# Performance work log

Hardware: AMD Instinct MI355X
Metric: run time of the kernel (lower is better)

The kernel has to match this reference:

```python
import jax, jax.numpy as jnp
import numpy as np

N = 100000
E = 3200000
D = 256
K = 1024
BETA = 1.0
LAMBDA_GRAPH = 0.1
ALPHA = 0.5
NUM_ITER = 2
LN_EPS = 1e-5


def setup_inputs() -> dict:
    key = jax.random.key(0)
    k1, k2, k3 = jax.random.split(key, 3)
    x = jax.random.normal(k1, (N, D), dtype=jnp.float32)
    edge_index = jax.random.randint(k2, (2, E), 0, N, dtype=jnp.int64)
    memory = jax.random.normal(k3, (K, D), dtype=jnp.float32) * 0.02  # memory patterns M [K, d]
    ln_gamma = jnp.ones((D,), dtype=jnp.float32)
    ln_beta = jnp.zeros((D,), dtype=jnp.float32)
    return {"x": x, "edge_index": edge_index, "memory": memory,
            "ln_gamma": ln_gamma, "ln_beta": ln_beta}


def _layer_norm(x, gamma, beta):
    mu = jnp.mean(x, axis=-1, keepdims=True)
    var = jnp.mean(jnp.square(x - mu), axis=-1, keepdims=True)
    return (x - mu) * jax.lax.rsqrt(var + LN_EPS) * gamma + beta


def _laplacian_term(x, row, col):
    # symmetric normalized Laplacian: x - D^{-1/2} A D^{-1/2} x
    deg = jax.ops.segment_sum(jnp.ones((E,), x.dtype), col, num_segments=N)  # [N]
    deg_inv_sqrt = jnp.where(deg > 0, jax.lax.rsqrt(jnp.maximum(deg, 1.0)), 0.0)
    norm_x = deg_inv_sqrt[:, None] * x                                        # [N, d]
    agg = jax.ops.segment_sum(norm_x[col], row, num_segments=N)               # scatter-add
    return x - deg_inv_sqrt[:, None] * agg


def reference(x, edge_index, memory, ln_gamma, ln_beta):
    row, col = edge_index[0], edge_index[1]
    lap_coeff = 2.0 * LAMBDA_GRAPH
    for _ in range(NUM_ITER):
        # Hopfield retrieval: softmax(beta * x M^T) M
        attn = jax.nn.softmax(BETA * jnp.einsum('nd,kd->nk', x, memory), axis=-1)
        retrieved = jnp.einsum('nk,kd->nd', attn, memory)
        lap = _laplacian_term(x, row, col)
        x_new = (1.0 - ALPHA) * x + ALPHA * (retrieved - lap_coeff * lap)
        x = _layer_norm(x_new, ln_gamma, ln_beta)
    return x
```

## Files before the change

### kernel.cpp

```cpp
#include <hip/hip_runtime.h>

#define DD 256
#define BSHIFT 9
#define BROWS  512
#define NBMAX  1024

typedef short bf16x8 __attribute__((ext_vector_type(8)));
typedef float f32x4 __attribute__((ext_vector_type(4)));

__device__ __forceinline__ float bf2f(ushort v) {
    union { uint u; float f; } c; c.u = ((uint)v) << 16; return c.f;
}
__device__ __forceinline__ ushort f2bf(float f) {
    union { float f; uint u; } c; c.f = f;
    uint u = c.u;
    u += 0x7fffu + ((u >> 16) & 1u);
    return (ushort)(u >> 16);
}

__global__ __launch_bounds__(256) void detect_kernel(const ushort* __restrict__ xbits,
                                                     const int* __restrict__ ei,
                                                     int* __restrict__ flags) {
    __shared__ int cnt[2];
    int t = threadIdx.x;
    if (t < 2) cnt[t] = 0;
    __syncthreads();
    int e = (xbits[2 * t] >> 7) & 0xFF;
    if (e >= 96 && e <= 144) atomicAdd(&cnt[0], 1);
    if (t < 128 && ei[2 * t + 1] == 0) atomicAdd(&cnt[1], 1);
    __syncthreads();
    if (t == 0) {
        flags[0] = (cnt[0] < 180) ? 1 : 0;
        flags[1] = (cnt[1] > 64) ? 1 : 0;
    }
}

__global__ void conv_bf_kernel(const void* __restrict__ src, ushort* __restrict__ dst,
                               int n, const int* __restrict__ flags) {
    int i = blockIdx.x * blockDim.x + threadIdx.x;
    if (i < n)
        dst[i] = flags[0] ? f2bf(((const float*)src)[i]) : ((const ushort*)src)[i];
}

__global__ void conv_f32_kernel(const void* __restrict__ src, float* __restrict__ dst,
                                int n, const int* __restrict__ flags) {
    int i = blockIdx.x * blockDim.x + threadIdx.x;
    if (i < n)
        dst[i] = flags[0] ? ((const float*)src)[i] : bf2f(((const ushort*)src)[i]);
}

__device__ __forceinline__ int edge_row(const int* ei, int e, int E_, int is64) {
    return ei[is64 ? (2 * e) : e];
}
__device__ __forceinline__ int edge_col(const int* ei, int e, int E_, int is64) {
    return ei[is64 ? (2 * (E_ + e)) : (E_ + e)];
}

__global__ __launch_bounds__(256) void countA_kernel(
        const int* __restrict__ ei, int E_, int n,
        int* __restrict__ colcnt, int* __restrict__ bkt_cnt,
        const int* __restrict__ flags) {
    __shared__ int hist[NBMAX];
    int t = threadIdx.x;
    for (int j = t; j < NBMAX; j += 256) hist[j] = 0;
    __syncthreads();
    int is64 = flags[1];
    int b0 = blockIdx.x * 4096;
    int bend = min(b0 + 4096, E_);
    for (int i = b0 + t; i < bend; i += 256) {
        int r = edge_row(ei, i, E_, is64);
        int c = edge_col(ei, i, E_, is64);
        if ((unsigned)r < (unsigned)n && (unsigned)c < (unsigned)n) {
            atomicAdd(&colcnt[c], 1);
            atomicAdd(&hist[r >> BSHIFT], 1);
        }
    }
    __syncthreads();
    for (int j = t; j < NBMAX; j += 256)
        if (hist[j] > 0) atomicAdd(&bkt_cnt[j], hist[j]);
}

__global__ void dinv_kernel(const int* __restrict__ colcnt, float* __restrict__ dinv, int n) {
    int i = blockIdx.x * blockDim.x + threadIdx.x;
    if (i < n) {
        int c = colcnt[i];
        dinv[i] = (c > 0) ? rsqrtf((float)c) : 0.0f;
    }
}

__global__ __launch_bounds__(1024) void bscan_kernel(
        const int* __restrict__ bkt_cnt, int* __restrict__ bbase,
        int* __restrict__ gcur, int nb) {
    __shared__ int lds[NBMAX];
    int t = threadIdx.x;
    int v = (t < nb) ? bkt_cnt[t] : 0;
    lds[t] = v;
    __syncthreads();
    for (int off = 1; off < NBMAX; off <<= 1) {
        int add = (t >= off) ? lds[t - off] : 0;
        __syncthreads();
        lds[t] += add;
        __syncthreads();
    }
    if (t < nb) {
        int base = lds[t] - v;
        bbase[t] = base;
        gcur[t]  = base;
    }
    if (t == nb - 1) bbase[nb] = lds[t];
}

__global__ __launch_bounds__(256) void partition_kernel(
        const int* __restrict__ ei, int E_, int n,
        int* __restrict__ gcur, uint2* __restrict__ pairs,
        const int* __restrict__ flags) {
    __shared__ int hist[NBMAX];
    __shared__ int base[NBMAX];
    int t = threadIdx.x;
    for (int j = t; j < NBMAX; j += 256) hist[j] = 0;
    __syncthreads();
    int is64 = flags[1];
    int b0 = blockIdx.x * 4096;
    int bend = min(b0 + 4096, E_);
    for (int i = b0 + t; i < bend; i += 256) {
        int r = edge_row(ei, i, E_, is64);
        int c = edge_col(ei, i, E_, is64);
        if ((unsigned)r < (unsigned)n && (unsigned)c < (unsigned)n)
            atomicAdd(&hist[r >> BSHIFT], 1);
    }
    __syncthreads();
    for (int j = t; j < NBMAX; j += 256) {
        int h = hist[j];
        base[j] = h ? atomicAdd(&gcur[j], h) : 0;
        hist[j] = 0;
    }
    __syncthreads();
    for (int i = b0 + t; i < bend; i += 256) {
        int r = edge_row(ei, i, E_, is64);
        int c = edge_col(ei, i, E_, is64);
        if ((unsigned)r < (unsigned)n && (unsigned)c < (unsigned)n) {
            int bk = r >> BSHIFT;
            int pos = base[bk] + atomicAdd(&hist[bk], 1);
            if ((unsigned)pos < (unsigned)E_)
                pairs[pos] = make_uint2((uint)r, (uint)c);
        }
    }
}

__global__ __launch_bounds__(1024) void place_kernel(
        const uint2* __restrict__ pairs, const int* __restrict__ bbase,
        int nb, int n, int E_, int* __restrict__ rowptr, int* __restrict__ csr) {
    __shared__ int hist[BROWS];
    __shared__ int scn[BROWS];
    __shared__ int cur[BROWS];
    int b = blockIdx.x;
    int t = threadIdx.x;
    int r0 = b << BSHIFT;
    int rows = min(BROWS, n - r0);
    int beg = bbase[b], end = bbase[b + 1];
    if (t < BROWS) hist[t] = 0;
    __syncthreads();
    for (int i = beg + t; i < end; i += 1024) {
        int lr = (int)pairs[i].x - r0;
        if ((unsigned)lr < (unsigned)BROWS) atomicAdd(&hist[lr], 1);
    }
    __syncthreads();
    int v = (t < BROWS) ? hist[t] : 0;
    if (t < BROWS) scn[t] = v;
    __syncthreads();
    for (int off = 1; off < BROWS; off <<= 1) {
        int add = (t < BROWS && t >= off) ? scn[t - off] : 0;
        __syncthreads();
        if (t < BROWS) scn[t] += add;
        __syncthreads();
    }
    if (t < rows) rowptr[r0 + t] = beg + scn[t] - v;
    if (b == nb - 1 && t == 0) rowptr[n] = end;
    if (t < BROWS) cur[t] = scn[t] - v;
    __syncthreads();
    for (int i = beg + t; i < end; i += 1024) {
        uint2 p = pairs[i];
        int lr = (int)p.x - r0;
        if ((unsigned)lr < (unsigned)BROWS) {
            int local = atomicAdd(&cur[lr], 1);
            int pos = beg + local;
            if ((unsigned)pos < (unsigned)E_)
                csr[pos] = (int)p.y;
        }
    }
}

__global__ void transpose_kernel(const ushort* __restrict__ M, ushort* __restrict__ Mt, int kdim) {
    int i = blockIdx.x * blockDim.x + threadIdx.x;
    if (i < kdim * DD) {
        int k = i >> 8, d = i & 255;
        Mt[(size_t)d * kdim + k] = M[i];
    }
}

__global__ __launch_bounds__(256) void lap_kernel(
    const ushort* __restrict__ xin,
    const int* __restrict__ rowptr, const int* __restrict__ csr,
    const float* __restrict__ dinv,
    ushort* __restrict__ agg, int n)
{
    __shared__ int   sc[256];
    __shared__ float sw[256];
    __shared__ float sacc[8][256];

    int r = blockIdx.x;
    int t = threadIdx.x;
    int slot = t >> 5, sub = t & 31;
    int beg = rowptr[r], end = rowptr[r + 1];
    int deg = (end > beg) ? (end - beg) : 0;

    float acc[8];
#pragma unroll
    for (int q = 0; q < 8; ++q) acc[q] = 0.0f;

    for (int base = 0; base < deg; base += 256) {
        int nb = min(256, deg - base);
        __syncthreads();
        if (t < nb) {
            int c = csr[beg + base + t];
            if ((unsigned)c >= (unsigned)n) c = 0;
            sc[t] = c;
            sw[t] = dinv[c];
        }
        __syncthreads();
        for (int j = slot; j < nb; j += 8) {
            int c = sc[j];
            float wgt = sw[j];
            bf16x8 v = *(const bf16x8*)(xin + (size_t)c * DD + sub * 8);
#pragma unroll
            for (int q = 0; q < 8; ++q) acc[q] += wgt * bf2f((ushort)v[q]);
        }
    }

#pragma unroll
    for (int q = 0; q < 8; ++q) sacc[slot][sub * 8 + q] = acc[q];
    __syncthreads();
    float s = 0.0f;
#pragma unroll
    for (int q = 0; q < 8; ++q) s += sacc[q][t];
    agg[(size_t)r * DD + t] = f2bf(s);
}

__global__ __launch_bounds__(256) void attn_fused_kernel(
    const ushort* __restrict__ x, const ushort* __restrict__ M,
    const ushort* __restrict__ Mt, const ushort* __restrict__ agg,
    const float* __restrict__ dinv,
    const float* __restrict__ gf, const float* __restrict__ bfa,
    void* __restrict__ out, int nrows, int kdim,
    int final_stage, const int* __restrict__ flags)
{
    __shared__ __align__(16) ushort Ml[32][DD + 8];
    __shared__ __align__(16) ushort Mtl[DD][32 + 8];
    __shared__ __align__(16) ushort Pl[4][16][32 + 8];

    const int tid  = threadIdx.x;
    const int wave = tid >> 6, lane = tid & 63;
    const int quad = lane >> 4, l16 = lane & 15;
    const int row0 = blockIdx.x * 64 + wave * 16;
    const int write_f32 = final_stage ? flags[0] : 0;

    bf16x8 afrag[8];
    {
        int r = row0 + l16;
        if (r < nrows) {
            const bf16x8* xr = (const bf16x8*)(x + (size_t)r * DD);
#pragma unroll
            for (int c = 0; c < 8; ++c) afrag[c] = xr[c * 4 + quad];
        } else {
#pragma unroll
            for (int c = 0; c < 8; ++c) afrag[c] = (bf16x8){0,0,0,0,0,0,0,0};
        }
    }

    float lsum[4] = {0.f, 0.f, 0.f, 0.f};
    f32x4 O[16];
#pragma unroll
    for (int i = 0; i < 16; ++i) O[i] = (f32x4){0.f, 0.f, 0.f, 0.f};

    const int nblk = kdim >> 5;
    for (int nb = 0; nb < nblk; ++nb) {
        __syncthreads();
#pragma unroll
        for (int it = 0; it < 4; ++it) {
            int i = tid + it * 256;
            int rr = i >> 5, cc = i & 31;
            *(uint4*)&Ml[rr][cc * 8] =
                *(const uint4*)(M + (size_t)(nb * 32 + rr) * DD + cc * 8);
        }
#pragma unroll
        for (int it = 0; it < 4; ++it) {
            int i = tid + it * 256;
            int rr = i >> 2, cc = i & 3;
            *(uint4*)&Mtl[rr][cc * 8] =
                *(const uint4*)(Mt + (size_t)rr * kdim + nb * 32 + cc * 8);
        }
        __syncthreads();

#pragma unroll
        for (int cc = 0; cc < 2; ++cc) {
            f32x4 s = (f32x4){0.f, 0.f, 0.f, 0.f};
#pragma unroll
            for (int ds = 0; ds < 8; ++ds) {
                bf16x8 b = *(const bf16x8*)&Ml[cc * 16 + l16][ds * 32 + quad * 8];
                s = __builtin_amdgcn_mfma_f32_16x16x32_bf16(afrag[ds], b, s, 0, 0, 0);
            }
#pragma unroll
            for (int rg = 0; rg < 4; ++rg) {
                float p = __expf(s[rg]);
                lsum[rg] += p;
                Pl[wave][quad * 4 + rg][cc * 16 + l16] = f2bf(p);
            }
        }
        __syncthreads();

        bf16x8 pa = *(const bf16x8*)&Pl[wave][l16][quad * 8];
#pragma unroll
        for (int f = 0; f < 16; ++f) {
            bf16x8 b = *(const bf16x8*)&Mtl[f * 16 + l16][quad * 8];
            O[f] = __builtin_amdgcn_mfma_f32_16x16x32_bf16(pa, b, O[f], 0, 0, 0);
        }
    }

    float l_r[4];
#pragma unroll
    for (int rg = 0; rg < 4; ++rg) {
        float v = lsum[rg];
#pragma unroll
        for (int off = 1; off < 16; off <<= 1) v += __shfl_xor(v, off);
        l_r[rg] = v;
    }

    float gcol[16], bcol[16];
#pragma unroll
    for (int f = 0; f < 16; ++f) {
        gcol[f] = gf[f * 16 + l16];
        bcol[f] = bfa[f * 16 + l16];
    }
#pragma unroll
    for (int rg = 0; rg < 4; ++rg) {
        int grow = row0 + quad * 4 + rg;
        if (grow < nrows) {
            float inv = 1.0f / l_r[rg];
            float dr  = dinv[grow];
            const ushort* xp = x   + (size_t)grow * DD;
            const ushort* ap = agg + (size_t)grow * DD;
            float xn[16];
            float s = 0.0f;
#pragma unroll
            for (int f = 0; f < 16; ++f) {
                float xr  = bf2f(xp[f * 16 + l16]);
                float ag  = bf2f(ap[f * 16 + l16]);
                float rv  = O[f][rg] * inv;
                float lap = xr - dr * ag;
                float v   = 0.5f * xr + 0.5f * (rv - 0.2f * lap);
                xn[f] = v;
                s += v;
            }
#pragma unroll
            for (int off = 1; off < 16; off <<= 1) s += __shfl_xor(s, off);
            float mu = s * (1.0f / 256.0f);
            float vs = 0.0f;
#pragma unroll
            for (int f = 0; f < 16; ++f) { float d = xn[f] - mu; vs += d * d; }
#pragma unroll
            for (int off = 1; off < 16; off <<= 1) vs += __shfl_xor(vs, off);
            float rstd = rsqrtf(vs * (1.0f / 256.0f) + 1e-5f);
            if (write_f32) {
                float* op = (float*)out + (size_t)grow * DD;
#pragma unroll
                for (int f = 0; f < 16; ++f)
                    op[f * 16 + l16] = (xn[f] - mu) * rstd * gcol[f] + bcol[f];
            } else {
                ushort* op = (ushort*)out + (size_t)grow * DD;
#pragma unroll
                for (int f = 0; f < 16; ++f)
                    op[f * 16 + l16] = f2bf((xn[f] - mu) * rstd * gcol[f] + bcol[f]);
            }
        }
    }
}

extern "C" void kernel_launch(void* const* d_in, const int* in_sizes, int n_in,
                              void* d_out, int out_size, void* d_ws, size_t ws_size,
                              hipStream_t stream)
{
    const void* x_raw = d_in[0];
    const int*  ei    = (const int*)d_in[1];
    const void* M_raw = d_in[2];
    const void* g_raw = d_in[3];
    const void* b_raw = d_in[4];

    const int N_ = in_sizes[0] / DD;
    const int E_ = in_sizes[1] / 2;
    const int K_ = in_sizes[2] / DD;
    const int NB_ = (N_ + BROWS - 1) >> BSHIFT;

    char* w = (char*)d_ws;
    size_t off = 0;
    auto alloc = [&](size_t bytes) -> char* {
        char* p = w + off;
        off = (off + bytes + 255) & ~(size_t)255;
        return p;
    };
    ushort* xbf     = (ushort*)alloc((size_t)N_ * DD * 2);
    ushort* agg     = (ushort*)alloc((size_t)N_ * DD * 2);
    int*    csr     = (int*)   alloc((size_t)E_ * 4);
    ushort* Mbf     = (ushort*)alloc((size_t)K_ * DD * 2);
    ushort* Mt      = (ushort*)alloc((size_t)K_ * DD * 2);
    float*  dinv    = (float*) alloc((size_t)N_ * 4);
    int*    colcnt  = (int*)   alloc((size_t)N_ * 4);
    int*    rowptr  = (int*)   alloc((size_t)(N_ + 1) * 4);
    float*  gf      = (float*) alloc((size_t)DD * 4);
    float*  bfa     = (float*) alloc((size_t)DD * 4);
    int*    flags   = (int*)   alloc(256);
    int*    bkt_cnt = (int*)   alloc((size_t)NBMAX * 4);
    int*    bbase   = (int*)   alloc((size_t)(NBMAX + 1) * 4);
    int*    gcur    = (int*)   alloc((size_t)NBMAX * 4);

    uint2* pairs = (uint2*)agg;

    hipMemsetAsync(colcnt, 0, (size_t)N_ * 4, stream);
    hipMemsetAsync(bkt_cnt, 0, (size_t)NBMAX * 4, stream);

    detect_kernel<<<1, 256, 0, stream>>>((const ushort*)x_raw, ei, flags);

    int nx = N_ * DD, nm = K_ * DD;
    conv_bf_kernel<<<(nx + 255) / 256, 256, 0, stream>>>(x_raw, xbf, nx, flags);
    conv_bf_kernel<<<(nm + 255) / 256, 256, 0, stream>>>(M_raw, Mbf, nm, flags);
    conv_f32_kernel<<<1, 256, 0, stream>>>(g_raw, gf, DD, flags);
    conv_f32_kernel<<<1, 256, 0, stream>>>(b_raw, bfa, DD, flags);
    transpose_kernel<<<(nm + 255) / 256, 256, 0, stream>>>(Mbf, Mt, K_);

    int gA = (E_ + 4095) / 4096;
    int gN = (N_ + 255) / 256;
    countA_kernel<<<gA, 256, 0, stream>>>(ei, E_, N_, colcnt, bkt_cnt, flags);
    dinv_kernel<<<gN, 256, 0, stream>>>(colcnt, dinv, N_);
    bscan_kernel<<<1, NBMAX, 0, stream>>>(bkt_cnt, bbase, gcur, NB_);
    partition_kernel<<<gA, 256, 0, stream>>>(ei, E_, N_, gcur, pairs, flags);
    place_kernel<<<NB_, 1024, 0, stream>>>(pairs, bbase, NB_, N_, E_, rowptr, csr);

    int attnBlocks = (N_ + 63) / 64;
    lap_kernel<<<N_, 256, 0, stream>>>(xbf, rowptr, csr, dinv, agg, N_);
    attn_fused_kernel<<<attnBlocks, 256, 0, stream>>>(xbf, Mbf, Mt, agg, dinv, gf, bfa,
                                                      (void*)xbf, N_, K_, 0, flags);
    lap_kernel<<<N_, 256, 0, stream>>>(xbf, rowptr, csr, dinv, agg, N_);
    attn_fused_kernel<<<attnBlocks, 256, 0, stream>>>(xbf, Mbf, Mt, agg, dinv, gf, bfa,
                                                      d_out, N_, K_, 1, flags);
}
```

Before: 1.373 ms.

## Load memory-pattern MFMA operands directly from global, drop LDS staging and block barriers

The attention kernel no longer stages M and Mt tiles into shared memory. Each wave reads its MFMA B operands straight from global memory, relying on L1/L2 because the 1024x256 bf16 memory matrix is small and shared by every block. The P tile becomes double-buffered per wave, and the two block-wide __syncthreads are replaced by a waitcnt plus scheduling barrier, since only intra-wave LDS exchange remains. This removes barrier stalls and LDS copy traffic at the cost of more global and cache load instructions, with more exposed latency per MFMA.

```diff
diff --git a/kernel.cpp b/kernel.cpp
--- a/kernel.cpp
+++ b/kernel.cpp
@@ -254,9 +254,7 @@
     void* __restrict__ out, int nrows, int kdim,
     int final_stage, const int* __restrict__ flags)
 {
-    __shared__ __align__(16) ushort Ml[32][DD + 8];
-    __shared__ __align__(16) ushort Mtl[DD][32 + 8];
-    __shared__ __align__(16) ushort Pl[4][16][32 + 8];
+    __shared__ __align__(16) ushort Pl[2][4][16][32 + 8];
 
     const int tid  = threadIdx.x;
     const int wave = tid >> 6, lane = tid & 63;
@@ -283,45 +281,32 @@
     for (int i = 0; i < 16; ++i) O[i] = (f32x4){0.f, 0.f, 0.f, 0.f};
 
     const int nblk = kdim >> 5;
+    const ushort* mtb = Mt + (size_t)l16 * kdim + quad * 8;
     for (int nb = 0; nb < nblk; ++nb) {
-        __syncthreads();
-#pragma unroll
-        for (int it = 0; it < 4; ++it) {
-            int i = tid + it * 256;
-            int rr = i >> 5, cc = i & 31;
-            *(uint4*)&Ml[rr][cc * 8] =
-                *(const uint4*)(M + (size_t)(nb * 32 + rr) * DD + cc * 8);
-        }
-#pragma unroll
-        for (int it = 0; it < 4; ++it) {
-            int i = tid + it * 256;
-            int rr = i >> 2, cc = i & 3;
-            *(uint4*)&Mtl[rr][cc * 8] =
-                *(const uint4*)(Mt + (size_t)rr * kdim + nb * 32 + cc * 8);
-        }
-        __syncthreads();
-
+        const int pb = nb & 1;
 #pragma unroll
         for (int cc = 0; cc < 2; ++cc) {
+            const ushort* mb = M + (size_t)(nb * 32 + cc * 16 + l16) * DD + quad * 8;
             f32x4 s = (f32x4){0.f, 0.f, 0.f, 0.f};
 #pragma unroll
             for (int ds = 0; ds < 8; ++ds) {
-                bf16x8 b = *(const bf16x8*)&Ml[cc * 16 + l16][ds * 32 + quad * 8];
+                bf16x8 b = *(const bf16x8*)(mb + ds * 32);
                 s = __builtin_amdgcn_mfma_f32_16x16x32_bf16(afrag[ds], b, s, 0, 0, 0);
             }
 #pragma unroll
             for (int rg = 0; rg < 4; ++rg) {
                 float p = __expf(s[rg]);
                 lsum[rg] += p;
-                Pl[wave][quad * 4 + rg][cc * 16 + l16] = f2bf(p);
+                Pl[pb][wave][quad * 4 + rg][cc * 16 + l16] = f2bf(p);
             }
         }
-        __syncthreads();
-
-        bf16x8 pa = *(const bf16x8*)&Pl[wave][l16][quad * 8];
+        asm volatile("s_waitcnt lgkmcnt(0)" ::: "memory");
+        __builtin_amdgcn_sched_barrier(0);
+        bf16x8 pa = *(const bf16x8*)&Pl[pb][wave][l16][quad * 8];
+        const ushort* mtc = mtb + nb * 32;
 #pragma unroll
         for (int f = 0; f < 16; ++f) {
-            bf16x8 b = *(const bf16x8*)&Mtl[f * 16 + l16][quad * 8];
+            bf16x8 b = *(const bf16x8*)(mtc + (size_t)(f * 16) * kdim);
             O[f] = __builtin_amdgcn_mfma_f32_16x16x32_bf16(pa, b, O[f], 0, 0, 0);
         }
     }
```

New measurement: 2.488 ms. 1.81x slower.

## Process two 16-row groups per wave in fused attention to reuse memory tiles

Applied to the files above, without the earlier changes.

Each wave in the fused Hopfield attention kernel now computes 32 rows instead of 16, so every 64-row half of a block shares the memory-pattern tiles staged in LDS. This halves the global and LDS traffic for M and Mt per output row. The block-wide barrier between writing and reading the probability tile is replaced by a per-wave LDS wait, since each wave owns its own probability buffer. The cost is roughly twice the accumulator registers, which risks spills or lower occupancy, and half as many blocks, which gives fewer waves to hide latency.

```diff
diff --git a/kernel.cpp b/kernel.cpp
--- a/kernel.cpp
+++ b/kernel.cpp
@@ -246,7 +246,7 @@
     agg[(size_t)r * DD + t] = f2bf(s);
 }
 
-__global__ __launch_bounds__(256) void attn_fused_kernel(
+__global__ __launch_bounds__(256, 2) void attn_fused_kernel(
     const ushort* __restrict__ x, const ushort* __restrict__ M,
     const ushort* __restrict__ Mt, const ushort* __restrict__ agg,
     const float* __restrict__ dinv,
@@ -256,31 +256,36 @@
 {
     __shared__ __align__(16) ushort Ml[32][DD + 8];
     __shared__ __align__(16) ushort Mtl[DD][32 + 8];
-    __shared__ __align__(16) ushort Pl[4][16][32 + 8];
+    __shared__ __align__(16) ushort Pl[4][2][16][32 + 8];
 
     const int tid  = threadIdx.x;
     const int wave = tid >> 6, lane = tid & 63;
     const int quad = lane >> 4, l16 = lane & 15;
-    const int row0 = blockIdx.x * 64 + wave * 16;
+    const int base_row = blockIdx.x * 128;
     const int write_f32 = final_stage ? flags[0] : 0;
 
-    bf16x8 afrag[8];
-    {
-        int r = row0 + l16;
+    bf16x8 afrag[2][8];
+#pragma unroll
+    for (int h = 0; h < 2; ++h) {
+        int r = base_row + h * 64 + wave * 16 + l16;
         if (r < nrows) {
             const bf16x8* xr = (const bf16x8*)(x + (size_t)r * DD);
 #pragma unroll
-            for (int c = 0; c < 8; ++c) afrag[c] = xr[c * 4 + quad];
+            for (int c = 0; c < 8; ++c) afrag[h][c] = xr[c * 4 + quad];
         } else {
 #pragma unroll
-            for (int c = 0; c < 8; ++c) afrag[c] = (bf16x8){0,0,0,0,0,0,0,0};
-        }
-    }
-
-    float lsum[4] = {0.f, 0.f, 0.f, 0.f};
-    f32x4 O[16];
-#pragma unroll
-    for (int i = 0; i < 16; ++i) O[i] = (f32x4){0.f, 0.f, 0.f, 0.f};
+            for (int c = 0; c < 8; ++c) afrag[h][c] = (bf16x8){0,0,0,0,0,0,0,0};
+        }
+    }
+
+    float lsum[2][4];
+#pragma unroll
+    for (int h = 0; h < 2; ++h)
+#pragma unroll
+        for (int rg = 0; rg < 4; ++rg) lsum[h][rg] = 0.f;
+    f32x4 O0[16], O1[16];
+#pragma unroll
+    for (int i = 0; i < 16; ++i) { O0[i] = (f32x4){0.f,0.f,0.f,0.f}; O1[i] = (f32x4){0.f,0.f,0.f,0.f}; }
 
     const int nblk = kdim >> 5;
     for (int nb = 0; nb < nblk; ++nb) {
@@ -303,36 +308,34 @@
 
 #pragma unroll
         for (int cc = 0; cc < 2; ++cc) {
-            f32x4 s = (f32x4){0.f, 0.f, 0.f, 0.f};
+            f32x4 s0 = (f32x4){0.f,0.f,0.f,0.f};
+            f32x4 s1 = (f32x4){0.f,0.f,0.f,0.f};
 #pragma unroll
             for (int ds = 0; ds < 8; ++ds) {
                 bf16x8 b = *(const bf16x8*)&Ml[cc * 16 + l16][ds * 32 + quad * 8];
-                s = __builtin_amdgcn_mfma_f32_16x16x32_bf16(afrag[ds], b, s, 0, 0, 0);
+                s0 = __builtin_amdgcn_mfma_f32_16x16x32_bf16(afrag[0][ds], b, s0, 0, 0, 0);
+                s1 = __builtin_amdgcn_mfma_f32_16x16x32_bf16(afrag[1][ds], b, s1, 0, 0, 0);
             }
 #pragma unroll
             for (int rg = 0; rg < 4; ++rg) {
-                float p = __expf(s[rg]);
-                lsum[rg] += p;
-                Pl[wave][quad * 4 + rg][cc * 16 + l16] = f2bf(p);
+                float p0 = __expf(s0[rg]);
+                float p1 = __expf(s1[rg]);
+                lsum[0][rg] += p0;
+                lsum[1][rg] += p1;
+                Pl[wave][0][quad * 4 + rg][cc * 16 + l16] = f2bf(p0);
+                Pl[wave][1][quad * 4 + rg][cc * 16 + l16] = f2bf(p1);
             }
         }
-        __syncthreads();
-
-        bf16x8 pa = *(const bf16x8*)&Pl[wave][l16][quad * 8];
+        asm volatile("s_waitcnt lgkmcnt(0)" ::: "memory");
+        __builtin_amdgcn_sched_barrier(0);
+        bf16x8 pa0 = *(const bf16x8*)&Pl[wave][0][l16][quad * 8];
+        bf16x8 pa1 = *(const bf16x8*)&Pl[wave][1][l16][quad * 8];
 #pragma unroll
         for (int f = 0; f < 16; ++f) {
             bf16x8 b = *(const bf16x8*)&Mtl[f * 16 + l16][quad * 8];
-            O[f] = __builtin_amdgcn_mfma_f32_16x16x32_bf16(pa, b, O[f], 0, 0, 0);
-        }
-    }
-
-    float l_r[4];
-#pragma unroll
-    for (int rg = 0; rg < 4; ++rg) {
-        float v = lsum[rg];
-#pragma unroll
-        for (int off = 1; off < 16; off <<= 1) v += __shfl_xor(v, off);
-        l_r[rg] = v;
+            O0[f] = __builtin_amdgcn_mfma_f32_16x16x32_bf16(pa0, b, O0[f], 0, 0, 0);
+            O1[f] = __builtin_amdgcn_mfma_f32_16x16x32_bf16(pa1, b, O1[f], 0, 0, 0);
+        }
     }
 
     float gcol[16], bcol[16];
@@ -342,44 +345,55 @@
         bcol[f] = bfa[f * 16 + l16];
     }
 #pragma unroll
-    for (int rg = 0; rg < 4; ++rg) {
-        int grow = row0 + quad * 4 + rg;
-        if (grow < nrows) {
-            float inv = 1.0f / l_r[rg];
-            float dr  = dinv[grow];
-            const ushort* xp = x   + (size_t)grow * DD;
-            const ushort* ap = agg + (size_t)grow * DD;
-            float xn[16];
-            float s = 0.0f;
-#pragma unroll
-            for (int f = 0; f < 16; ++f) {
-                float xr  = bf2f(xp[f * 16 + l16]);
-                float ag  = bf2f(ap[f * 16 + l16]);
-                float rv  = O[f][rg] * inv;
-                float lap = xr - dr * ag;
-                float v   = 0.5f * xr + 0.5f * (rv - 0.2f * lap);
-                xn[f] = v;
-                s += v;
-            }
-#pragma unroll
-            for (int off = 1; off < 16; off <<= 1) s += __shfl_xor(s, off);
-            float mu = s * (1.0f / 256.0f);
-            float vs = 0.0f;
-#pragma unroll
-            for (int f = 0; f < 16; ++f) { float d = xn[f] - mu; vs += d * d; }
-#pragma unroll
-            for (int off = 1; off < 16; off <<= 1) vs += __shfl_xor(vs, off);
-            float rstd = rsqrtf(vs * (1.0f / 256.0f) + 1e-5f);
-            if (write_f32) {
-                float* op = (float*)out + (size_t)grow * DD;
-#pragma unroll
-                for (int f = 0; f < 16; ++f)
-                    op[f * 16 + l16] = (xn[f] - mu) * rstd * gcol[f] + bcol[f];
-            } else {
-                ushort* op = (ushort*)out + (size_t)grow * DD;
-#pragma unroll
-                for (int f = 0; f < 16; ++f)
-                    op[f * 16 + l16] = f2bf((xn[f] - mu) * rstd * gcol[f] + bcol[f]);
+    for (int h = 0; h < 2; ++h) {
+        float l_r[4];
+#pragma unroll
+        for (int rg = 0; rg < 4; ++rg) {
+            float v = lsum[h][rg];
+#pragma unroll
+            for (int off = 1; off < 16; off <<= 1) v += __shfl_xor(v, off);
+            l_r[rg] = v;
+        }
+#pragma unroll
+        for (int rg = 0; rg < 4; ++rg) {
+            int grow = base_row + h * 64 + wave * 16 + quad * 4 + rg;
+            if (grow < nrows) {
+                float inv = 1.0f / l_r[rg];
+                float dr  = dinv[grow];
+                const ushort* xp = x   + (size_t)grow * DD;
+                const ushort* ap = agg + (size_t)grow * DD;
+                float xn[16];
+                float s = 0.0f;
+#pragma unroll
+                for (int f = 0; f < 16; ++f) {
+                    float xr  = bf2f(xp[f * 16 + l16]);
+                    float ag  = bf2f(ap[f * 16 + l16]);
+                    float rv  = (h ? O1[f][rg] : O0[f][rg]) * inv;
+                    float lap = xr - dr * ag;
+                    float v   = 0.5f * xr + 0.5f * (rv - 0.2f * lap);
+                    xn[f] = v;
+                    s += v;
+                }
+#pragma unroll
+                for (int off = 1; off < 16; off <<= 1) s += __shfl_xor(s, off);
+                float mu = s * (1.0f / 256.0f);
+                float vs = 0.0f;
+#pragma unroll
+                for (int f = 0; f < 16; ++f) { float d = xn[f] - mu; vs += d * d; }
+#pragma unroll
+                for (int off = 1; off < 16; off <<= 1) vs += __shfl_xor(vs, off);
+                float rstd = rsqrtf(vs * (1.0f / 256.0f) + 1e-5f);
+                if (write_f32) {
+                    float* op = (float*)out + (size_t)grow * DD;
+#pragma unroll
+                    for (int f = 0; f < 16; ++f)
+                        op[f * 16 + l16] = (xn[f] - mu) * rstd * gcol[f] + bcol[f];
+                } else {
+                    ushort* op = (ushort*)out + (size_t)grow * DD;
+#pragma unroll
+                    for (int f = 0; f < 16; ++f)
+                        op[f * 16 + l16] = f2bf((xn[f] - mu) * rstd * gcol[f] + bcol[f]);
+                }
             }
         }
     }
@@ -444,7 +458,7 @@
     partition_kernel<<<gA, 256, 0, stream>>>(ei, E_, N_, gcur, pairs, flags);
     place_kernel<<<NB_, 1024, 0, stream>>>(pairs, bbase, NB_, N_, E_, rowptr, csr);
 
-    int attnBlocks = (N_ + 63) / 64;
+    int attnBlocks = (N_ + 127) / 128;
     lap_kernel<<<N_, 256, 0, stream>>>(xbf, rowptr, csr, dinv, agg, N_);
     attn_fused_kernel<<<attnBlocks, 256, 0, stream>>>(xbf, Mbf, Mt, agg, dinv, gf, bfa,
                                                       (void*)xbf, N_, K_, 0, flags);
```

Result: no change. 1.373 ms (-0.0%).
